# Performance work log

Hardware: AMD Instinct MI355X
Metric: run time of the kernel (lower is better)

The kernel has to match this reference:

```python
import jax, jax.numpy as jnp
import numpy as np

B, S, H = 4, 2048, 2048
E, K = 8, 2


def setup_inputs() -> dict:
    key = jax.random.key(0)
    k1, k2, k3 = jax.random.split(key, 3)
    hidden_states = jax.random.normal(k1, (B, S, H), dtype=jnp.float32)
    # torch nn.Linear weight layout: [out_features, in_features]
    gate_w = jax.random.normal(k2, (E, H), dtype=jnp.float32) * (1.0 / np.sqrt(H))
    expert_w = jax.random.normal(k3, (E, H, H), dtype=jnp.float32) * (1.0 / np.sqrt(H))
    return {"hidden_states": hidden_states, "gate_w": gate_w, "expert_w": expert_w}


def reference(hidden_states, gate_w, expert_w):
    b, s, h = hidden_states.shape
    x = hidden_states.reshape(-1, h)                      # [T, H]
    T = x.shape[0]
    router_logits = x @ gate_w.T                          # [T, E]
    probs = jax.nn.softmax(router_logits.astype(jnp.float32), axis=-1)
    topk_w, topk_idx = jax.lax.top_k(probs, K)            # [T, K]
    topk_w = topk_w / jnp.sum(topk_w, axis=-1, keepdims=True)  # norm_topk_prob
    topk_w = topk_w.astype(x.dtype)
    # dense combine weights: cw[t, e] = sum_k topk_w[t, k] * (topk_idx[t, k] == e)
    cw = jnp.zeros((T, E), dtype=x.dtype).at[jnp.arange(T)[:, None], topk_idx].add(topk_w)
    # per-expert outputs: expert e computes x @ W_e^T  (W_e is [out, in])
    expert_out = jnp.einsum('th,edh->ted', x, expert_w)   # [T, E, H]
    out = jnp.einsum('ted,te->td', expert_out, cw)        # [T, H]
    return out.reshape(b, s, h), router_logits
```

## Files before the change

### kernel.cpp

```cpp
#include <hip/hip_runtime.h>
#include <hip/hip_bf16.h>

#define T_TOK 8192
#define H_DIM 2048
#define NE 8

typedef float f32x4 __attribute__((ext_vector_type(4)));
typedef short s16x8 __attribute__((ext_vector_type(8)));

typedef __attribute__((address_space(3))) unsigned int lds_uint;
typedef __attribute__((address_space(1))) const unsigned int glob_uint;

static __device__ __forceinline__ void async_ld16(const void* g, void* l) {
    __builtin_amdgcn_global_load_lds((glob_uint*)g, (lds_uint*)l, 16, 0, 0);
}

static __device__ __forceinline__ unsigned short f32_to_bf16(float f) {
    unsigned int u = __builtin_bit_cast(unsigned int, f);
    unsigned int r = (u + 0x7FFFu + ((u >> 16) & 1u)) >> 16;
    return (unsigned short)r;
}

__global__ __launch_bounds__(256) void prep_kernel(
        const float* __restrict__ w, unsigned short* __restrict__ wb,
        int* __restrict__ cnt) {
    const long g = (long)blockIdx.x * 256 + threadIdx.x;
    if (g < NE) cnt[g] = 0;
    const long nt = (long)gridDim.x * 256;
    const long N_W4 = (long)NE * H_DIM * H_DIM / 4;
    const float4* w4 = (const float4*)w;
    ushort4* wb4 = (ushort4*)wb;
    for (long i = g; i < N_W4; i += nt) {
        float4 v = w4[i];
        wb4[i] = make_ushort4(f32_to_bf16(v.x), f32_to_bf16(v.y),
                              f32_to_bf16(v.z), f32_to_bf16(v.w));
    }
}

__global__ __launch_bounds__(256) void router_kernel(
        const float* __restrict__ x, const float* __restrict__ gate,
        unsigned short* __restrict__ xb, float* __restrict__ logits,
        int* __restrict__ cnt, int* __restrict__ list, float* __restrict__ wl) {
    __shared__ float4 gs[NE * H_DIM / 4];
    __shared__ int aExp[32];
    __shared__ float aW[32];
    const float4* g4 = (const float4*)gate;
    for (int i = threadIdx.x; i < NE * H_DIM / 4; i += 256) gs[i] = g4[i];
    __syncthreads();

    const int wave = threadIdx.x >> 6, lane = threadIdx.x & 63;

    for (int it = 0; it < 4; ++it) {
        const int tok = wave * 4 + it;
        const int t = blockIdx.x * 16 + tok;
        const float4* xr = (const float4*)(x + (long)t * H_DIM);
        ushort4* xw = (ushort4*)(xb + (long)t * H_DIM);
        float acc[NE];
#pragma unroll
        for (int e = 0; e < NE; ++e) acc[e] = 0.f;
#pragma unroll
        for (int i = 0; i < 8; ++i) {
            float4 xv = xr[i * 64 + lane];
            xw[i * 64 + lane] = make_ushort4(f32_to_bf16(xv.x), f32_to_bf16(xv.y),
                                             f32_to_bf16(xv.z), f32_to_bf16(xv.w));
#pragma unroll
            for (int e = 0; e < NE; ++e) {
                float4 gv = gs[e * 512 + i * 64 + lane];
                acc[e] += xv.x * gv.x + xv.y * gv.y + xv.z * gv.z + xv.w * gv.w;
            }
        }
#pragma unroll
        for (int e = 0; e < NE; ++e)
#pragma unroll
            for (int off = 32; off > 0; off >>= 1)
                acc[e] += __shfl_xor(acc[e], off, 64);

        if (lane == 0) {
            float l0 = -1e30f; int i0 = 0;
#pragma unroll
            for (int e = 0; e < NE; ++e)
                if (acc[e] > l0) { l0 = acc[e]; i0 = e; }
            float l1 = -1e30f; int i1 = 0;
#pragma unroll
            for (int e = 0; e < NE; ++e)
                if (e != i0 && acc[e] > l1) { l1 = acc[e]; i1 = e; }
            float e1v = __expf(l1 - l0);
            float inv = 1.f / (1.f + e1v);
#pragma unroll
            for (int e = 0; e < NE; ++e) logits[(long)t * NE + e] = acc[e];
            aExp[tok * 2] = i0;     aW[tok * 2] = inv;
            aExp[tok * 2 + 1] = i1; aW[tok * 2 + 1] = e1v * inv;
        }
    }
    __syncthreads();

    if (threadIdx.x < NE) {
        const int e = threadIdx.x;
        int c = 0;
#pragma unroll
        for (int k = 0; k < 32; ++k) c += (aExp[k] == e);
        if (c) {
            int pos = atomicAdd(&cnt[e], c);
            for (int k = 0; k < 32; ++k)
                if (aExp[k] == e) {
                    list[e * T_TOK + pos] = blockIdx.x * 16 + (k >> 1);
                    wl[e * T_TOK + pos] = aW[k];
                    ++pos;
                }
        }
    }
}

__global__ __launch_bounds__(256, 4) void moe_gemm(
        const unsigned short* __restrict__ xb, const unsigned short* __restrict__ wb,
        const int* __restrict__ cnt, const int* __restrict__ list,
        const float* __restrict__ wl, float* __restrict__ out) {
    __shared__ uint4 As[1024];
    __shared__ uint4 Bs[1024];
    __shared__ int tIdx[128];
    __shared__ float tw[128];

    const int bx = blockIdx.x;
    const int e  = bx >> 10;
    const int rt = (bx >> 4) & 63;
    const int ct = bx & 15;
    const int n = cnt[e];
    const int row0 = rt << 7;
    if (row0 >= n) return;
    const int rv = min(128, n - row0);

    const int tid = threadIdx.x;
    if (tid < 128) {
        if (tid < rv) {
            tIdx[tid] = list[e * T_TOK + row0 + tid];
            tw[tid]   = wl[e * T_TOK + row0 + tid];
        } else { tIdx[tid] = 0; tw[tid] = 0.f; }
    }
    __syncthreads();

    const int wave = tid >> 6, lane = tid & 63;
    const int wm = (wave >> 1) << 6;
    const int wn = (wave & 1) << 6;
    const int quad = lane >> 4, l16 = lane & 15;

    f32x4 acc[4][4];
#pragma unroll
    for (int i = 0; i < 4; ++i)
#pragma unroll
        for (int j = 0; j < 4; ++j) acc[i][j] = (f32x4){0.f, 0.f, 0.f, 0.f};

    const unsigned short* aSrc[4];
    const unsigned short* bSrc[4];
    const long wbase = (long)e * H_DIM * H_DIM + (long)(ct * 128) * H_DIM;
#pragma unroll
    for (int i = 0; i < 4; ++i) {
        const int p = i * 256 + wave * 64 + lane;
        const int r = p >> 3;
        const int c = (p & 7) ^ (r & 7);
        aSrc[i] = xb + (long)tIdx[r] * H_DIM + c * 8;
        bSrc[i] = wb + wbase + (long)r * H_DIM + c * 8;
    }

    for (int kt = 0; kt < H_DIM / 64; ++kt) {
        const int k0 = kt * 64;
#pragma unroll
        for (int i = 0; i < 4; ++i) {
            async_ld16(aSrc[i] + k0, &As[i * 256 + wave * 64]);
            async_ld16(bSrc[i] + k0, &Bs[i * 256 + wave * 64]);
        }
        __syncthreads();
#pragma unroll
        for (int ks = 0; ks < 2; ++ks) {
            s16x8 af[4], bfr[4];
            const int kc = ks * 4 + quad;
#pragma unroll
            for (int i = 0; i < 4; ++i) {
                int r = wm + i * 16 + l16;
                af[i] = ((const s16x8*)As)[(r << 3) | (kc ^ (r & 7))];
            }
#pragma unroll
            for (int j = 0; j < 4; ++j) {
                int d = wn + j * 16 + l16;
                bfr[j] = ((const s16x8*)Bs)[(d << 3) | (kc ^ (d & 7))];
            }
#pragma unroll
            for (int i = 0; i < 4; ++i)
#pragma unroll
                for (int j = 0; j < 4; ++j)
                    acc[i][j] = __builtin_amdgcn_mfma_f32_16x16x32_bf16(
                        af[i], bfr[j], acc[i][j], 0, 0, 0);
        }
        __syncthreads();
    }

    const int colbase = ct * 128 + wn;
#pragma unroll
    for (int i = 0; i < 4; ++i) {
        const int rbase = wm + i * 16 + quad * 4;
#pragma unroll
        for (int jr = 0; jr < 4; ++jr) {
            const int r = rbase + jr;
            if (r < rv) {
                const float wgt = tw[r];
                const long orow = (long)tIdx[r] * H_DIM + colbase;
#pragma unroll
                for (int j = 0; j < 4; ++j)
                    atomicAdd(&out[orow + j * 16 + l16], acc[i][j][jr] * wgt);
            }
        }
    }
}

extern "C" void kernel_launch(void* const* d_in, const int* in_sizes, int n_in,
                              void* d_out, int out_size, void* d_ws, size_t ws_size,
                              hipStream_t stream) {
    (void)in_sizes; (void)n_in; (void)out_size; (void)ws_size;
    const float* x    = (const float*)d_in[0];
    const float* gate = (const float*)d_in[1];
    const float* w    = (const float*)d_in[2];

    float* out    = (float*)d_out;
    float* logits = out + (size_t)T_TOK * H_DIM;

    char* ws = (char*)d_ws;
    unsigned short* xb = (unsigned short*)(ws);
    unsigned short* wb = (unsigned short*)(ws + 33554432);
    int*   cnt  = (int*)(ws + 100663296);
    int*   list = (int*)(ws + 100663328);
    float* wl   = (float*)(ws + 100925472);

    hipMemsetAsync(out, 0, (size_t)T_TOK * H_DIM * sizeof(float), stream);
    prep_kernel<<<2048, 256, 0, stream>>>(w, wb, cnt);
    router_kernel<<<512, 256, 0, stream>>>(x, gate, xb, logits, cnt, list, wl);
    moe_gemm<<<8192, 256, 0, stream>>>(xb, wb, cnt, list, wl, out);
}
```

Baseline: 489.1 us.

## Fuse expert weight bf16 conversion into GEMM with register prefetch of B tiles

Drops the separate prep kernel that converted all expert weights to bf16. The GEMM now loads fp32 weights directly into registers one k-tile ahead, converts them to bf16 and stores them to LDS, while activations still use async global-to-LDS loads. This removes a full pass over the weights. In exchange each GEMM block re-reads and re-converts fp32 weights (twice the bytes per B tile), adds register pressure (launch bounds lowered to 3), and raises MFMA priority during compute.

```diff
diff --git a/kernel.cpp b/kernel.cpp
--- a/kernel.cpp
+++ b/kernel.cpp
@@ -4,6 +4,7 @@
 #define T_TOK 8192
 #define H_DIM 2048
 #define NE 8
+#define NT (H_DIM / 64)
 
 typedef float f32x4 __attribute__((ext_vector_type(4)));
 typedef short s16x8 __attribute__((ext_vector_type(8)));
@@ -21,20 +22,8 @@
     return (unsigned short)r;
 }
 
-__global__ __launch_bounds__(256) void prep_kernel(
-        const float* __restrict__ w, unsigned short* __restrict__ wb,
-        int* __restrict__ cnt) {
-    const long g = (long)blockIdx.x * 256 + threadIdx.x;
-    if (g < NE) cnt[g] = 0;
-    const long nt = (long)gridDim.x * 256;
-    const long N_W4 = (long)NE * H_DIM * H_DIM / 4;
-    const float4* w4 = (const float4*)w;
-    ushort4* wb4 = (ushort4*)wb;
-    for (long i = g; i < N_W4; i += nt) {
-        float4 v = w4[i];
-        wb4[i] = make_ushort4(f32_to_bf16(v.x), f32_to_bf16(v.y),
-                              f32_to_bf16(v.z), f32_to_bf16(v.w));
-    }
+static __device__ __forceinline__ unsigned int pack_bf16x2(float lo, float hi) {
+    return (unsigned int)f32_to_bf16(lo) | ((unsigned int)f32_to_bf16(hi) << 16);
 }
 
 __global__ __launch_bounds__(256) void router_kernel(
@@ -111,8 +100,8 @@
     }
 }
 
-__global__ __launch_bounds__(256, 4) void moe_gemm(
-        const unsigned short* __restrict__ xb, const unsigned short* __restrict__ wb,
+__global__ __launch_bounds__(256, 3) void moe_gemm(
+        const unsigned short* __restrict__ xb, const float* __restrict__ w,
         const int* __restrict__ cnt, const int* __restrict__ list,
         const float* __restrict__ wl, float* __restrict__ out) {
     __shared__ uint4 As[1024];
@@ -150,25 +139,56 @@
         for (int j = 0; j < 4; ++j) acc[i][j] = (f32x4){0.f, 0.f, 0.f, 0.f};
 
     const unsigned short* aSrc[4];
-    const unsigned short* bSrc[4];
+    const float* bSrc[4];
+    int bChunk[4];
     const long wbase = (long)e * H_DIM * H_DIM + (long)(ct * 128) * H_DIM;
 #pragma unroll
     for (int i = 0; i < 4; ++i) {
-        const int p = i * 256 + wave * 64 + lane;
+        const int p = i * 256 + tid;
         const int r = p >> 3;
         const int c = (p & 7) ^ (r & 7);
         aSrc[i] = xb + (long)tIdx[r] * H_DIM + c * 8;
-        bSrc[i] = wb + wbase + (long)r * H_DIM + c * 8;
-    }
-
-    for (int kt = 0; kt < H_DIM / 64; ++kt) {
+        bSrc[i] = w + wbase + (long)r * H_DIM + c * 8;
+        bChunk[i] = p;
+    }
+
+    float4 bPre[4][2];
+#pragma unroll
+    for (int i = 0; i < 4; ++i) {
+        const float4* s = (const float4*)bSrc[i];
+        bPre[i][0] = s[0];
+        bPre[i][1] = s[1];
+    }
+
+    for (int kt = 0; kt < NT; ++kt) {
         const int k0 = kt * 64;
+        __syncthreads();
+
+#pragma unroll
+        for (int i = 0; i < 4; ++i)
+            async_ld16(aSrc[i] + k0, &As[i * 256 + wave * 64]);
 #pragma unroll
         for (int i = 0; i < 4; ++i) {
-            async_ld16(aSrc[i] + k0, &As[i * 256 + wave * 64]);
-            async_ld16(bSrc[i] + k0, &Bs[i * 256 + wave * 64]);
-        }
-        __syncthreads();
+            uint4 o;
+            o.x = pack_bf16x2(bPre[i][0].x, bPre[i][0].y);
+            o.y = pack_bf16x2(bPre[i][0].z, bPre[i][0].w);
+            o.z = pack_bf16x2(bPre[i][1].x, bPre[i][1].y);
+            o.w = pack_bf16x2(bPre[i][1].z, bPre[i][1].w);
+            Bs[bChunk[i]] = o;
+        }
+        if (kt + 1 < NT) {
+#pragma unroll
+            for (int i = 0; i < 4; ++i) {
+                const float4* s = (const float4*)(bSrc[i] + k0 + 64);
+                bPre[i][0] = s[0];
+                bPre[i][1] = s[1];
+            }
+            asm volatile("s_waitcnt vmcnt(8) lgkmcnt(0)" ::: "memory");
+        } else {
+            asm volatile("s_waitcnt vmcnt(0) lgkmcnt(0)" ::: "memory");
+        }
+        __builtin_amdgcn_s_barrier();
+
 #pragma unroll
         for (int ks = 0; ks < 2; ++ks) {
             s16x8 af[4], bfr[4];
@@ -183,14 +203,15 @@
                 int d = wn + j * 16 + l16;
                 bfr[j] = ((const s16x8*)Bs)[(d << 3) | (kc ^ (d & 7))];
             }
+            __builtin_amdgcn_s_setprio(1);
 #pragma unroll
             for (int i = 0; i < 4; ++i)
 #pragma unroll
                 for (int j = 0; j < 4; ++j)
                     acc[i][j] = __builtin_amdgcn_mfma_f32_16x16x32_bf16(
                         af[i], bfr[j], acc[i][j], 0, 0, 0);
-        }
-        __syncthreads();
+            __builtin_amdgcn_s_setprio(0);
+        }
     }
 
     const int colbase = ct * 128 + wn;
@@ -224,13 +245,12 @@
 
     char* ws = (char*)d_ws;
     unsigned short* xb = (unsigned short*)(ws);
-    unsigned short* wb = (unsigned short*)(ws + 33554432);
     int*   cnt  = (int*)(ws + 100663296);
     int*   list = (int*)(ws + 100663328);
     float* wl   = (float*)(ws + 100925472);
 
     hipMemsetAsync(out, 0, (size_t)T_TOK * H_DIM * sizeof(float), stream);
-    prep_kernel<<<2048, 256, 0, stream>>>(w, wb, cnt);
+    hipMemsetAsync(cnt, 0, NE * sizeof(int), stream);
     router_kernel<<<512, 256, 0, stream>>>(x, gate, xb, logits, cnt, list, wl);
-    moe_gemm<<<8192, 256, 0, stream>>>(xb, wb, cnt, list, wl, out);
-}
+    moe_gemm<<<8192, 256, 0, stream>>>(xb, w, cnt, list, wl, out);
+}
```

Result: slower. 523.9 us (+7.1%).
